# Performance work log

Hardware: AMD Instinct MI355X
Metric: run time of the kernel (lower is better)

Reference implementation:

```python
import jax, jax.numpy as jnp
import numpy as np

EPS = 1e-5

def conv2d(x, w, b=None, pad=1):
    # x: [B,C,H,W], w: [O,I,kh,kw]
    y = jax.lax.conv_general_dilated(x, w, (1, 1), [(pad, pad), (pad, pad)],
                                     dimension_numbers=('NCHW', 'OIHW', 'NCHW'))
    if b is not None:
        y = y + b[None, :, None, None]
    return y

def bn(x, g, b, m, v):
    # inference-mode batchnorm
    inv = g / jnp.sqrt(v + EPS)
    return x * inv[None, :, None, None] + (b - m * inv)[None, :, None, None]

def coord_conv(x, w, b):
    B, C, H, W = x.shape
    yy = jnp.broadcast_to(jnp.linspace(-1.0, 1.0, H)[:, None], (H, W))
    xx = jnp.broadcast_to(jnp.linspace(-1.0, 1.0, W)[None, :], (H, W))
    coords = jnp.broadcast_to(jnp.stack([xx, yy])[None], (B, 2, H, W)).astype(x.dtype)
    return conv2d(jnp.concatenate([x, coords], axis=1), w, b, pad=1)

def deform_conv(x, offset, w):
    # deformable conv v1, 3x3, pad=1, stride=1, no bias
    B, C, H, W = x.shape
    K = 9
    # offset channels interleaved (y, x) per kernel tap
    off = offset.reshape(B, K, 2, H, W)
    off_y, off_x = off[:, :, 0], off[:, :, 1]          # [B,9,H,W]
    k = jnp.arange(K)
    ko_y = (k // 3 - 1).astype(x.dtype)[None, :, None, None]
    ko_x = (k % 3 - 1).astype(x.dtype)[None, :, None, None]
    base_y = jnp.arange(H, dtype=x.dtype)[None, None, :, None]
    base_x = jnp.arange(W, dtype=x.dtype)[None, None, None, :]
    py = base_y + ko_y + off_y                          # [B,9,H,W]
    px = base_x + ko_x + off_x
    xf = x.reshape(B, C, H * W)
    y0 = jnp.floor(py)
    x0 = jnp.floor(px)
    acc = jnp.zeros((B, C, K, H, W), x.dtype)
    for dy in (0.0, 1.0):
        for dx in (0.0, 1.0):
            yy = y0 + dy
            xx = x0 + dx
            wgt = (1.0 - jnp.abs(py - yy)) * (1.0 - jnp.abs(px - xx))
            valid = (yy >= 0) & (yy < H) & (xx >= 0) & (xx < W)
            wgt = jnp.where(valid, wgt, 0.0)            # zero padding OOB
            yi = jnp.clip(yy, 0, H - 1).astype(jnp.int32)
            xi = jnp.clip(xx, 0, W - 1).astype(jnp.int32)
            idx = (yi * W + xi).reshape(B, K * H * W)
            v = jnp.take_along_axis(xf, idx[:, None, :], axis=2).reshape(B, C, K, H, W)
            acc = acc + v * wgt[:, None]
    wk = w.reshape(w.shape[0], w.shape[1], K)           # [O,I,9]
    return jnp.einsum('bckhw,ock->bohw', acc, wk)

def setup_inputs() -> dict:
    key = jax.random.key(0)
    ks = jax.random.split(key, 16)
    d_model, hd = 256, 64
    B, H, W = 8, 96, 96
    f32 = jnp.float32
    def bn_params(k):
        k1, k2, k3 = jax.random.split(k, 3)
        return (1.0 + 0.1 * jax.random.normal(k1, (hd,), f32),
                0.1 * jax.random.normal(k2, (hd,), f32),
                0.1 * jax.random.normal(k3, (hd,), f32),
                0.5 + jax.random.uniform(jax.random.fold_in(k, 7), (hd,), f32))
    bn1 = bn_params(ks[1]); bn2 = bn_params(ks[2]); bn3 = bn_params(ks[3]); bn4 = bn_params(ks[4])
    inp = {
        'features': jax.random.normal(ks[0], (B, H, W, d_model), f32),
        'coord_w': 0.05 * jax.random.normal(ks[5], (hd, d_model + 2, 3, 3), f32),
        'coord_b': jnp.zeros((hd,), f32),
        'bn1_g': bn1[0], 'bn1_b': bn1[1], 'bn1_m': bn1[2], 'bn1_v': bn1[3],
        'off_w': 0.01 * jax.random.normal(ks[6], (18, hd, 3, 3), f32),
        'off_b': 0.01 * jax.random.normal(ks[7], (18,), f32),
        'dc_w': 0.05 * jax.random.normal(ks[8], (hd, hd, 3, 3), f32),
        'bn2_g': bn2[0], 'bn2_b': bn2[1], 'bn2_m': bn2[2], 'bn2_v': bn2[3],
        'r1_w': 0.05 * jax.random.normal(ks[9], (hd, hd, 3, 3), f32),
        'bn3_g': bn3[0], 'bn3_b': bn3[1], 'bn3_m': bn3[2], 'bn3_v': bn3[3],
        'r2_w': 0.05 * jax.random.normal(ks[10], (hd, hd, 3, 3), f32),
        'bn4_g': bn4[0], 'bn4_b': bn4[1], 'bn4_m': bn4[2], 'bn4_v': bn4[3],
        'out_w': 0.1 * jax.random.normal(ks[11], (1, hd, 1, 1), f32),
        'out_b': jnp.zeros((1,), f32),
    }
    return inp

def reference(features, coord_w, coord_b, bn1_g, bn1_b, bn1_m, bn1_v,
              off_w, off_b, dc_w, bn2_g, bn2_b, bn2_m, bn2_v,
              r1_w, bn3_g, bn3_b, bn3_m, bn3_v,
              r2_w, bn4_g, bn4_b, bn4_m, bn4_v, out_w, out_b):
    x = jnp.transpose(features, (0, 3, 1, 2))           # NHWC -> NCHW
    x = jax.nn.relu(bn(coord_conv(x, coord_w, coord_b), bn1_g, bn1_b, bn1_m, bn1_v))
    offset = conv2d(x, off_w, off_b, pad=1)
    x = deform_conv(x, offset, dc_w)
    x = jax.nn.relu(bn(x, bn2_g, bn2_b, bn2_m, bn2_v))
    x = jax.nn.relu(bn(conv2d(x, r1_w, None, pad=1), bn3_g, bn3_b, bn3_m, bn3_v))
    x = jax.nn.relu(bn(conv2d(x, r2_w, None, pad=1), bn4_g, bn4_b, bn4_m, bn4_v))
    return jax.nn.sigmoid(conv2d(x, out_w, out_b, pad=0))
```

## Files before the change

### kernel.cpp

```cpp
#include <hip/hip_runtime.h>


typedef unsigned short u16;
typedef unsigned int u32;
typedef __attribute__((ext_vector_type(8)))  short bf16x8;
typedef __attribute__((ext_vector_type(16))) float f32x16;

#define EPSBN 1e-5f

__device__ __forceinline__ u16 f2bf(float f) {
  u32 u = __builtin_bit_cast(u32, f);
  u32 r = u + 0x7FFFu + ((u >> 16) & 1u);
  return (u16)(r >> 16);
}
__device__ __forceinline__ u32 pk2(float a, float b) {
  return (u32)f2bf(a) | ((u32)f2bf(b) << 16);
}
__device__ __forceinline__ float lo2f(u32 w) { return __builtin_bit_cast(float, w << 16); }
__device__ __forceinline__ float hi2f(u32 w) { return __builtin_bit_cast(float, w & 0xFFFF0000u); }

#define N_WCF 147456
#define N_WCC 9216
#define N_WOF 18432
#define N_W64 36864
#define N_ALLW (N_WCF + N_WCC + N_WOF + 3*N_W64)

__global__ __launch_bounds__(256) void prep_kernel(
    const float* __restrict__ coord_w, const float* __restrict__ off_w,
    const float* __restrict__ dc_w, const float* __restrict__ r1_w,
    const float* __restrict__ r2_w,
    u16* __restrict__ wcf, u16* __restrict__ wcc, u16* __restrict__ wof,
    u16* __restrict__ wdf, u16* __restrict__ wr1, u16* __restrict__ wr2)
{
  int i = blockIdx.x * 256 + threadIdx.x;
  if (i >= N_ALLW) return;
  int d = i;
  if (d < N_WCF) {
    int j = d & 7, lane = (d >> 3) & 63, frag = d >> 9;
    int nt = frag & 1, h = (frag >> 1) & 3, tap = (frag >> 3) % 9, cc = (frag >> 3) / 9;
    int ic = cc * 64 + h * 16 + ((lane >> 5) << 3) + j;
    int oc = nt * 32 + (lane & 31);
    wcf[d] = f2bf(coord_w[((size_t)oc * 258 + ic) * 9 + tap]);
    return;
  }
  d -= N_WCF;
  if (d < N_WCC) {
    int j = d & 7, lane = (d >> 3) & 63, frag = d >> 9;
    int nt = frag & 1, tap = frag >> 1;
    int ic = 256 + ((lane >> 5) << 3) + j;
    int oc = nt * 32 + (lane & 31);
    wcc[d] = (ic < 258) ? f2bf(coord_w[((size_t)oc * 258 + ic) * 9 + tap]) : (u16)0;
    return;
  }
  d -= N_WCC;
  if (d < N_WOF) {
    int j = d & 7, lane = (d >> 3) & 63, frag = d >> 9;
    int h = frag & 3, tap = frag >> 2;
    int ic = h * 16 + ((lane >> 5) << 3) + j;
    int oc = lane & 31;
    wof[d] = (oc < 18) ? f2bf(off_w[((size_t)oc * 64 + ic) * 9 + tap]) : (u16)0;
    return;
  }
  d -= N_WOF;
  int seg = d / N_W64;
  int e = d - seg * N_W64;
  int j = e & 7, lane = (e >> 3) & 63, frag = e >> 9;
  int nt = frag & 1, h = (frag >> 1) & 3, tap = frag >> 3;
  int ic = h * 16 + ((lane >> 5) << 3) + j;
  int oc = nt * 32 + (lane & 31);
  const float* src = (seg == 0) ? dc_w : (seg == 1) ? r1_w : r2_w;
  u16* dst = (seg == 0) ? wdf : (seg == 1) ? wr1 : wr2;
  dst[e] = f2bf(src[((size_t)oc * 64 + ic) * 9 + tap]);
}

__global__ __launch_bounds__(256, 3) void coord_conv_kernel(
    const float* __restrict__ feat, const u16* __restrict__ wcf,
    const u16* __restrict__ wcc, const float* __restrict__ cb,
    const float* __restrict__ g, const float* __restrict__ bb,
    const float* __restrict__ m, const float* __restrict__ v,
    u16* __restrict__ x1b)
{
  __shared__ __align__(16) u16 tile[6 * 34 * 72];
  const int t = threadIdx.x;
  const int wv = t >> 6, lane = t & 63;
  const int l31 = lane & 31, l5 = lane >> 5;
  const int x0 = blockIdx.x * 32, y0 = blockIdx.y * 4, b = blockIdx.z;

  f32x16 acc[2] = {};
  float4 pa[7], pb[7];

  auto issue = [&](int cc) {
    #pragma unroll
    for (int r = 0; r < 7; ++r) {
      const int i = t + r * 256;
      const float4 z = {0.f, 0.f, 0.f, 0.f};
      pa[r] = z; pb[r] = z;
      if (i < 1632) {
        const int px = i >> 3, gg = i & 7;
        const int ly = px / 34, lx = px - ly * 34;
        const int gy = y0 + ly - 1, gx = x0 + lx - 1;
        if ((unsigned)gy < 96u && (unsigned)gx < 96u) {
          const float* p = feat + ((size_t)((b * 96 + gy) * 96 + gx)) * 256
                           + cc * 64 + gg * 8;
          pa[r] = *(const float4*)p;
          pb[r] = *(const float4*)(p + 4);
        }
      }
    }
  };
  auto commit = [&]() {
    #pragma unroll
    for (int r = 0; r < 7; ++r) {
      const int i = t + r * 256;
      if (i < 1632) {
        const int px = i >> 3, gg = i & 7;
        uint4 o;
        o.x = pk2(pa[r].x, pa[r].y); o.y = pk2(pa[r].z, pa[r].w);
        o.z = pk2(pb[r].x, pb[r].y); o.w = pk2(pb[r].z, pb[r].w);
        *(uint4*)(tile + px * 72 + gg * 8) = o;
      }
    }
  };

  issue(0);
  for (int cc = 0; cc < 4; ++cc) {
    __syncthreads();
    commit();
    __syncthreads();
    if (cc < 3) issue(cc + 1);
    #pragma unroll
    for (int tap = 0; tap < 9; ++tap) {
      const int dy = tap / 3, dx = tap - dy * 3;
      #pragma unroll
      for (int h = 0; h < 4; ++h) {
        const bf16x8 afr = *(const bf16x8*)(tile +
            ((wv + dy) * 34 + l31 + dx) * 72 + h * 16 + l5 * 8);
        #pragma unroll
        for (int nt = 0; nt < 2; ++nt) {
          const bf16x8 bfr = *(const bf16x8*)(wcf +
              ((size_t)((((cc * 9 + tap) * 4 + h) * 2) + nt)) * 512 + lane * 8);
          acc[nt] = __builtin_amdgcn_mfma_f32_32x32x16_bf16(afr, bfr, acc[nt],
                                                            0, 0, 0);
        }
      }
    }
  }

  __syncthreads();
  for (int i = t; i < 408; i += 256) {
    const int px = i >> 1, gg = i & 1;
    const int ly = px / 34, lx = px - ly * 34;
    const int gy = y0 + ly - 1, gx = x0 + lx - 1;
    uint4 o = {0u, 0u, 0u, 0u};
    if (gg == 0 && (unsigned)gy < 96u && (unsigned)gx < 96u) {
      const float xx = -1.f + (2.f / 95.f) * (float)gx;
      const float yy = -1.f + (2.f / 95.f) * (float)gy;
      o.x = pk2(xx, yy);
    }
    *(uint4*)(tile + (ly * 34 + lx) * 72 + gg * 8) = o;
  }
  __syncthreads();
  #pragma unroll
  for (int tap = 0; tap < 9; ++tap) {
    const int dy = tap / 3, dx = tap - dy * 3;
    const bf16x8 afr = *(const bf16x8*)(tile +
        ((wv + dy) * 34 + l31 + dx) * 72 + l5 * 8);
    #pragma unroll
    for (int nt = 0; nt < 2; ++nt) {
      const bf16x8 bfr = *(const bf16x8*)(wcc +
          ((size_t)(tap * 2 + nt)) * 512 + lane * 8);
      acc[nt] = __builtin_amdgcn_mfma_f32_32x32x16_bf16(afr, bfr, acc[nt],
                                                        0, 0, 0);
    }
  }

  const int y = y0 + wv;
  #pragma unroll
  for (int nt = 0; nt < 2; ++nt) {
    const int oc = nt * 32 + l31;
    const float inv = g[oc] * rsqrtf(v[oc] + EPSBN);
    const float sh = bb[oc] - m[oc] * inv + cb[oc] * inv;
    #pragma unroll
    for (int r = 0; r < 16; ++r) {
      const int xr = (r & 3) + 8 * (r >> 2) + 4 * l5;
      const float val = fmaxf(fmaf(acc[nt][r], inv, sh), 0.f);
      x1b[((size_t)((b * 96 + y) * 96 + x0 + xr)) * 64 + oc] = f2bf(val);
    }
  }
}

template<int NN, int EPI>
__global__ __launch_bounds__(256, 4) void conv64_kernel(
    const u16* __restrict__ xin, const u16* __restrict__ wf,
    const float* __restrict__ bias,
    const float* __restrict__ g, const float* __restrict__ bb,
    const float* __restrict__ m, const float* __restrict__ v,
    const float* __restrict__ ow, const float* __restrict__ ob,
    void* __restrict__ outp)
{
  __shared__ __align__(16) u16 tile[6 * 34 * 72];
  __shared__ float red[128];
  const int t = threadIdx.x;
  const int wv = t >> 6, lane = t & 63;
  const int l31 = lane & 31, l5 = lane >> 5;
  const int x0 = blockIdx.x * 32, y0 = blockIdx.y * 4, b = blockIdx.z;

  uint4 pf[7];
  #pragma unroll
  for (int r = 0; r < 7; ++r) {
    const int i = t + r * 256;
    const uint4 z = {0u, 0u, 0u, 0u};
    pf[r] = z;
    if (i < 1632) {
      const int px = i >> 3, gg = i & 7;
      const int ly = px / 34, lx = px - ly * 34;
      const int gy = y0 + ly - 1, gx = x0 + lx - 1;
      if ((unsigned)gy < 96u && (unsigned)gx < 96u)
        pf[r] = *(const uint4*)(xin + (((size_t)((b * 96 + gy) * 96 + gx)) << 6)
                                + gg * 8);
    }
  }
  #pragma unroll
  for (int r = 0; r < 7; ++r) {
    const int i = t + r * 256;
    if (i < 1632) {
      const int px = i >> 3, gg = i & 7;
      *(uint4*)(tile + px * 72 + gg * 8) = pf[r];
    }
  }
  __syncthreads();

  f32x16 acc[NN] = {};
  #pragma unroll
  for (int tap = 0; tap < 9; ++tap) {
    const int dy = tap / 3, dx = tap - dy * 3;
    #pragma unroll
    for (int h = 0; h < 4; ++h) {
      const bf16x8 afr = *(const bf16x8*)(tile +
          ((wv + dy) * 34 + l31 + dx) * 72 + h * 16 + l5 * 8);
      #pragma unroll
      for (int nt = 0; nt < NN; ++nt) {
        const bf16x8 bfr = *(const bf16x8*)(wf +
            ((size_t)((tap * 4 + h) * NN + nt)) * 512 + lane * 8);
        acc[nt] = __builtin_amdgcn_mfma_f32_32x32x16_bf16(afr, bfr, acc[nt],
                                                          0, 0, 0);
      }
    }
  }

  const int y = y0 + wv;
  if constexpr (EPI == 0) {
    u16* xo = (u16*)outp;
    #pragma unroll
    for (int nt = 0; nt < NN; ++nt) {
      const int oc = nt * 32 + l31;
      const float inv = g[oc] * rsqrtf(v[oc] + EPSBN);
      const float sh = bb[oc] - m[oc] * inv;
      #pragma unroll
      for (int r = 0; r < 16; ++r) {
        const int xr = (r & 3) + 8 * (r >> 2) + 4 * l5;
        const float val = fmaxf(fmaf(acc[nt][r], inv, sh), 0.f);
        xo[((size_t)((b * 96 + y) * 96 + x0 + xr)) * 64 + oc] = f2bf(val);
      }
    }
  } else if constexpr (EPI == 1) {
    float* fo = (float*)outp;
    const int oc = l31;
    if (oc < 18) {
      const float bs = bias[oc];
      #pragma unroll
      for (int r = 0; r < 16; ++r) {
        const int xr = (r & 3) + 8 * (r >> 2) + 4 * l5;
        fo[((size_t)((b * 96 + y) * 96 + x0 + xr)) * 18 + oc] = acc[0][r] + bs;
      }
    }
  } else {
    float pr[16];
    #pragma unroll
    for (int r = 0; r < 16; ++r) pr[r] = 0.f;
    #pragma unroll
    for (int nt = 0; nt < NN; ++nt) {
      const int oc = nt * 32 + l31;
      const float inv = g[oc] * rsqrtf(v[oc] + EPSBN);
      const float sh = bb[oc] - m[oc] * inv;
      const float wo = ow[oc];
      #pragma unroll
      for (int r = 0; r < 16; ++r) {
        const float val = fmaxf(fmaf(acc[nt][r], inv, sh), 0.f);
        pr[r] = fmaf(val, wo, pr[r]);
      }
    }
    #pragma unroll
    for (int mask = 1; mask <= 16; mask <<= 1)
      #pragma unroll
      for (int r = 0; r < 16; ++r)
        pr[r] += __shfl_xor(pr[r], mask);
    if (l31 == 0) {
      #pragma unroll
      for (int r = 0; r < 16; ++r) {
        const int xr = (r & 3) + 8 * (r >> 2) + 4 * l5;
        red[wv * 32 + xr] = pr[r];
      }
    }
    __syncthreads();
    if (t < 128) {
      float* fo = (float*)outp;
      const int yy = y0 + (t >> 5), xx = x0 + (t & 31);
      const float val = red[t] + ob[0];
      fo[(size_t)(b * 96 + yy) * 96 + xx] = 1.f / (1.f + expf(-val));
    }
  }
}

__global__ __launch_bounds__(256, 4) void deform_kernel(
    const u16* __restrict__ x1b, const float* __restrict__ off,
    const u16* __restrict__ wdf,
    const float* __restrict__ g, const float* __restrict__ bb,
    const float* __restrict__ m, const float* __restrict__ v,
    u16* __restrict__ x2b)
{
  __shared__ __align__(16) u16 s[128 * 72];
  __shared__ float offs[128 * 18];
  const int t = threadIdx.x;
  const int wv = t >> 6, lane = t & 63;
  const int l31 = lane & 31, l5 = lane >> 5;
  const int x0 = blockIdx.x * 16, y0 = blockIdx.y * 8, b = blockIdx.z;

  {
    float po[9];
    #pragma unroll
    for (int r = 0; r < 9; ++r) {
      const int i = t + r * 256;
      const int p = i / 18, c = i - p * 18;
      const int gy = y0 + (p >> 4), gx = x0 + (p & 15);
      po[r] = off[((size_t)((b * 96 + gy) * 96 + gx)) * 18 + c];
    }
    #pragma unroll
    for (int r = 0; r < 9; ++r) offs[t + r * 256] = po[r];
  }

  f32x16 acc[2] = {};

  for (int k = 0; k < 9; ++k) {
    __syncthreads();
    #pragma unroll
    for (int rr = 0; rr < 2; ++rr) {
      const int role = t + rr * 256;
      const int sp = role >> 2, part = role & 3;
      const int sy = y0 + (sp >> 4), sx = x0 + (sp & 15);
      const float oy = offs[sp * 18 + 2 * k];
      const float ox = offs[sp * 18 + 2 * k + 1];
      const float py = (float)(sy + k / 3 - 1) + oy;
      const float px = (float)(sx + k % 3 - 1) + ox;
      const float yf = floorf(py), xf = floorf(px);
      const float fy = py - yf, fx = px - xf;
      const int yi = (int)yf, xi = (int)xf;
      float val[16];
      #pragma unroll
      for (int j = 0; j < 16; ++j) val[j] = 0.f;
      #pragma unroll
      for (int cor = 0; cor < 4; ++cor) {
        const int cy = yi + (cor >> 1), cx = xi + (cor & 1);
        if ((unsigned)cy < 96u && (unsigned)cx < 96u) {
          const float wy = (cor & 2) ? fy : 1.f - fy;
          const float wx = (cor & 1) ? fx : 1.f - fx;
          const float wgt = wy * wx;
          const u16* sp2 = x1b + ((size_t)((b * 96 + cy) * 96 + cx)) * 64
                           + part * 16;
          const uint4 ua = *(const uint4*)sp2;
          const uint4 ub = *(const uint4*)(sp2 + 8);
          const u32 uu[8] = {ua.x, ua.y, ua.z, ua.w, ub.x, ub.y, ub.z, ub.w};
          #pragma unroll
          for (int u = 0; u < 8; ++u) {
            val[2 * u]     = fmaf(wgt, lo2f(uu[u]), val[2 * u]);
            val[2 * u + 1] = fmaf(wgt, hi2f(uu[u]), val[2 * u + 1]);
          }
        }
      }
      u32 pk[8];
      #pragma unroll
      for (int u = 0; u < 8; ++u) pk[u] = pk2(val[2 * u], val[2 * u + 1]);
      uint4 w0 = {pk[0], pk[1], pk[2], pk[3]};
      uint4 w1 = {pk[4], pk[5], pk[6], pk[7]};
      *(uint4*)(s + sp * 72 + part * 16) = w0;
      *(uint4*)(s + sp * 72 + part * 16 + 8) = w1;
    }
    __syncthreads();
    #pragma unroll
    for (int h = 0; h < 4; ++h) {
      const bf16x8 afr = *(const bf16x8*)(s + (wv * 32 + l31) * 72
                                          + h * 16 + l5 * 8);
      #pragma unroll
      for (int nt = 0; nt < 2; ++nt) {
        const bf16x8 bfr = *(const bf16x8*)(wdf +
            ((size_t)((k * 4 + h) * 2 + nt)) * 512 + lane * 8);
        acc[nt] = __builtin_amdgcn_mfma_f32_32x32x16_bf16(afr, bfr, acc[nt],
                                                          0, 0, 0);
      }
    }
  }

  #pragma unroll
  for (int nt = 0; nt < 2; ++nt) {
    const int oc = nt * 32 + l31;
    const float inv = g[oc] * rsqrtf(v[oc] + EPSBN);
    const float sh = bb[oc] - m[oc] * inv;
    #pragma unroll
    for (int r = 0; r < 16; ++r) {
      const int pxi = wv * 32 + (r & 3) + 8 * (r >> 2) + 4 * l5;
      const int y = y0 + (pxi >> 4), x = x0 + (pxi & 15);
      const float val = fmaxf(fmaf(acc[nt][r], inv, sh), 0.f);
      x2b[((size_t)((b * 96 + y) * 96 + x)) * 64 + oc] = f2bf(val);
    }
  }
}

extern "C" void kernel_launch(void* const* d_in, const int* in_sizes, int n_in,
                              void* d_out, int out_size, void* d_ws,
                              size_t ws_size, hipStream_t stream)
{
  (void)in_sizes; (void)n_in; (void)out_size; (void)ws_size;
  const float* features = (const float*)d_in[0];
  const float* coord_w  = (const float*)d_in[1];
  const float* coord_b  = (const float*)d_in[2];
  const float* bn1g = (const float*)d_in[3];
  const float* bn1b = (const float*)d_in[4];
  const float* bn1m = (const float*)d_in[5];
  const float* bn1v = (const float*)d_in[6];
  const float* off_w = (const float*)d_in[7];
  const float* off_b = (const float*)d_in[8];
  const float* dc_w  = (const float*)d_in[9];
  const float* bn2g = (const float*)d_in[10];
  const float* bn2b = (const float*)d_in[11];
  const float* bn2m = (const float*)d_in[12];
  const float* bn2v = (const float*)d_in[13];
  const float* r1_w = (const float*)d_in[14];
  const float* bn3g = (const float*)d_in[15];
  const float* bn3b = (const float*)d_in[16];
  const float* bn3m = (const float*)d_in[17];
  const float* bn3v = (const float*)d_in[18];
  const float* r2_w = (const float*)d_in[19];
  const float* bn4g = (const float*)d_in[20];
  const float* bn4b = (const float*)d_in[21];
  const float* bn4m = (const float*)d_in[22];
  const float* bn4v = (const float*)d_in[23];
  const float* out_w = (const float*)d_in[24];
  const float* out_b = (const float*)d_in[25];

  char* W = (char*)d_ws;
  float* offb = (float*)W;
  u16*   x1b  = (u16*)(W + 5308416);
  u16*   x2b  = (u16*)(W + 14745600);
  u16*   x3b  = (u16*)(W + 24182784);
  u16*   wcf  = (u16*)(W + 33619968);
  u16*   wcc  = wcf + N_WCF;
  u16*   wof  = wcc + N_WCC;
  u16*   wdf  = wof + N_WOF;
  u16*   wr1  = wdf + N_W64;
  u16*   wr2  = wr1 + N_W64;

  prep_kernel<<<(N_ALLW + 255) / 256, 256, 0, stream>>>(
      coord_w, off_w, dc_w, r1_w, r2_w, wcf, wcc, wof, wdf, wr1, wr2);

  dim3 grid(3, 24, 8);
  dim3 gridD(6, 12, 8);

  coord_conv_kernel<<<grid, 256, 0, stream>>>(
      features, wcf, wcc, coord_b, bn1g, bn1b, bn1m, bn1v, x1b);
  conv64_kernel<1, 1><<<grid, 256, 0, stream>>>(
      x1b, wof, off_b, nullptr, nullptr, nullptr, nullptr, nullptr, nullptr,
      (void*)offb);
  deform_kernel<<<gridD, 256, 0, stream>>>(
      x1b, offb, wdf, bn2g, bn2b, bn2m, bn2v, x2b);
  conv64_kernel<2, 0><<<grid, 256, 0, stream>>>(
      x2b, wr1, nullptr, bn3g, bn3b, bn3m, bn3v, nullptr, nullptr, (void*)x3b);
  conv64_kernel<2, 2><<<grid, 256, 0, stream>>>(
      x3b, wr2, nullptr, bn4g, bn4b, bn4m, bn4v, out_w, out_b, d_out);
}
```

Baseline: 259.7 us.

## Double wavefronts per block, split output channels across waves, pipeline deform gathers

```diff
diff --git a/kernel.cpp b/kernel.cpp
--- a/kernel.cpp
+++ b/kernel.cpp
@@ -73,7 +73,7 @@
   dst[e] = f2bf(src[((size_t)oc * 64 + ic) * 9 + tap]);
 }
 
-__global__ __launch_bounds__(256, 3) void coord_conv_kernel(
+__global__ __launch_bounds__(512, 4) void coord_conv_kernel(
     const float* __restrict__ feat, const u16* __restrict__ wcf,
     const u16* __restrict__ wcc, const float* __restrict__ cb,
     const float* __restrict__ g, const float* __restrict__ bb,
@@ -84,15 +84,16 @@
   const int t = threadIdx.x;
   const int wv = t >> 6, lane = t & 63;
   const int l31 = lane & 31, l5 = lane >> 5;
+  const int row = wv & 3, ntw = wv >> 2;
   const int x0 = blockIdx.x * 32, y0 = blockIdx.y * 4, b = blockIdx.z;
 
-  f32x16 acc[2] = {};
-  float4 pa[7], pb[7];
+  f32x16 acc = {};
+  float4 pa[4], pb[4];
 
   auto issue = [&](int cc) {
     #pragma unroll
-    for (int r = 0; r < 7; ++r) {
-      const int i = t + r * 256;
+    for (int r = 0; r < 4; ++r) {
+      const int i = t + r * 512;
       const float4 z = {0.f, 0.f, 0.f, 0.f};
       pa[r] = z; pb[r] = z;
       if (i < 1632) {
@@ -110,8 +111,8 @@
   };
   auto commit = [&]() {
     #pragma unroll
-    for (int r = 0; r < 7; ++r) {
-      const int i = t + r * 256;
+    for (int r = 0; r < 4; ++r) {
+      const int i = t + r * 512;
       if (i < 1632) {
         const int px = i >> 3, gg = i & 7;
         uint4 o;
@@ -134,20 +135,16 @@
       #pragma unroll
       for (int h = 0; h < 4; ++h) {
         const bf16x8 afr = *(const bf16x8*)(tile +
-            ((wv + dy) * 34 + l31 + dx) * 72 + h * 16 + l5 * 8);
-        #pragma unroll
-        for (int nt = 0; nt < 2; ++nt) {
-          const bf16x8 bfr = *(const bf16x8*)(wcf +
-              ((size_t)((((cc * 9 + tap) * 4 + h) * 2) + nt)) * 512 + lane * 8);
-          acc[nt] = __builtin_amdgcn_mfma_f32_32x32x16_bf16(afr, bfr, acc[nt],
-                                                            0, 0, 0);
-        }
+            ((row + dy) * 34 + l31 + dx) * 72 + h * 16 + l5 * 8);
+        const bf16x8 bfr = *(const bf16x8*)(wcf +
+            ((size_t)((((cc * 9 + tap) * 4 + h) * 2) + ntw)) * 512 + lane * 8);
+        acc = __builtin_amdgcn_mfma_f32_32x32x16_bf16(afr, bfr, acc, 0, 0, 0);
       }
     }
   }
 
   __syncthreads();
-  for (int i = t; i < 408; i += 256) {
+  for (int i = t; i < 408; i += 512) {
     const int px = i >> 1, gg = i & 1;
     const int ly = px / 34, lx = px - ly * 34;
     const int gy = y0 + ly - 1, gx = x0 + lx - 1;
@@ -164,33 +161,26 @@
   for (int tap = 0; tap < 9; ++tap) {
     const int dy = tap / 3, dx = tap - dy * 3;
     const bf16x8 afr = *(const bf16x8*)(tile +
-        ((wv + dy) * 34 + l31 + dx) * 72 + l5 * 8);
-    #pragma unroll
-    for (int nt = 0; nt < 2; ++nt) {
-      const bf16x8 bfr = *(const bf16x8*)(wcc +
-          ((size_t)(tap * 2 + nt)) * 512 + lane * 8);
-      acc[nt] = __builtin_amdgcn_mfma_f32_32x32x16_bf16(afr, bfr, acc[nt],
-                                                        0, 0, 0);
-    }
-  }
-
-  const int y = y0 + wv;
+        ((row + dy) * 34 + l31 + dx) * 72 + l5 * 8);
+    const bf16x8 bfr = *(const bf16x8*)(wcc +
+        ((size_t)(tap * 2 + ntw)) * 512 + lane * 8);
+    acc = __builtin_amdgcn_mfma_f32_32x32x16_bf16(afr, bfr, acc, 0, 0, 0);
+  }
+
+  const int y = y0 + row;
+  const int oc = ntw * 32 + l31;
+  const float inv = g[oc] * rsqrtf(v[oc] + EPSBN);
+  const float sh = bb[oc] - m[oc] * inv + cb[oc] * inv;
   #pragma unroll
-  for (int nt = 0; nt < 2; ++nt) {
-    const int oc = nt * 32 + l31;
-    const float inv = g[oc] * rsqrtf(v[oc] + EPSBN);
-    const float sh = bb[oc] - m[oc] * inv + cb[oc] * inv;
-    #pragma unroll
-    for (int r = 0; r < 16; ++r) {
-      const int xr = (r & 3) + 8 * (r >> 2) + 4 * l5;
-      const float val = fmaxf(fmaf(acc[nt][r], inv, sh), 0.f);
-      x1b[((size_t)((b * 96 + y) * 96 + x0 + xr)) * 64 + oc] = f2bf(val);
-    }
+  for (int r = 0; r < 16; ++r) {
+    const int xr = (r & 3) + 8 * (r >> 2) + 4 * l5;
+    const float val = fmaxf(fmaf(acc[r], inv, sh), 0.f);
+    x1b[((size_t)((b * 96 + y) * 96 + x0 + xr)) * 64 + oc] = f2bf(val);
   }
 }
 
 template<int NN, int EPI>
-__global__ __launch_bounds__(256, 4) void conv64_kernel(
+__global__ __launch_bounds__(512, 4) void conv64_kernel(
     const u16* __restrict__ xin, const u16* __restrict__ wf,
     const float* __restrict__ bias,
     const float* __restrict__ g, const float* __restrict__ bb,
@@ -199,16 +189,17 @@
     void* __restrict__ outp)
 {
   __shared__ __align__(16) u16 tile[6 * 34 * 72];
-  __shared__ float red[128];
+  __shared__ float red[2][128];
   const int t = threadIdx.x;
   const int wv = t >> 6, lane = t & 63;
   const int l31 = lane & 31, l5 = lane >> 5;
+  const int row = wv & 3, ntw = wv >> 2;
   const int x0 = blockIdx.x * 32, y0 = blockIdx.y * 4, b = blockIdx.z;
 
-  uint4 pf[7];
+  uint4 pf[4];
   #pragma unroll
-  for (int r = 0; r < 7; ++r) {
-    const int i = t + r * 256;
+  for (int r = 0; r < 4; ++r) {
+    const int i = t + r * 512;
     const uint4 z = {0u, 0u, 0u, 0u};
     pf[r] = z;
     if (i < 1632) {
@@ -221,8 +212,8 @@
     }
   }
   #pragma unroll
-  for (int r = 0; r < 7; ++r) {
-    const int i = t + r * 256;
+  for (int r = 0; r < 4; ++r) {
+    const int i = t + r * 512;
     if (i < 1632) {
       const int px = i >> 3, gg = i & 7;
       *(uint4*)(tile + px * 72 + gg * 8) = pf[r];
@@ -230,63 +221,80 @@
   }
   __syncthreads();
 
-  f32x16 acc[NN] = {};
+  f32x16 acc = {};
   #pragma unroll
   for (int tap = 0; tap < 9; ++tap) {
     const int dy = tap / 3, dx = tap - dy * 3;
-    #pragma unroll
-    for (int h = 0; h < 4; ++h) {
-      const bf16x8 afr = *(const bf16x8*)(tile +
-          ((wv + dy) * 34 + l31 + dx) * 72 + h * 16 + l5 * 8);
-      #pragma unroll
-      for (int nt = 0; nt < NN; ++nt) {
+    if constexpr (NN == 2) {
+      #pragma unroll
+      for (int h = 0; h < 4; ++h) {
+        const bf16x8 afr = *(const bf16x8*)(tile +
+            ((row + dy) * 34 + l31 + dx) * 72 + h * 16 + l5 * 8);
         const bf16x8 bfr = *(const bf16x8*)(wf +
-            ((size_t)((tap * 4 + h) * NN + nt)) * 512 + lane * 8);
-        acc[nt] = __builtin_amdgcn_mfma_f32_32x32x16_bf16(afr, bfr, acc[nt],
-                                                          0, 0, 0);
-      }
-    }
-  }
-
-  const int y = y0 + wv;
+            ((size_t)((tap * 4 + h) * 2 + ntw)) * 512 + lane * 8);
+        acc = __builtin_amdgcn_mfma_f32_32x32x16_bf16(afr, bfr, acc, 0, 0, 0);
+      }
+    } else {
+      #pragma unroll
+      for (int hh = 0; hh < 2; ++hh) {
+        const int h = ntw * 2 + hh;
+        const bf16x8 afr = *(const bf16x8*)(tile +
+            ((row + dy) * 34 + l31 + dx) * 72 + h * 16 + l5 * 8);
+        const bf16x8 bfr = *(const bf16x8*)(wf +
+            ((size_t)(tap * 4 + h)) * 512 + lane * 8);
+        acc = __builtin_amdgcn_mfma_f32_32x32x16_bf16(afr, bfr, acc, 0, 0, 0);
+      }
+    }
+  }
+
+  const int y = y0 + row;
   if constexpr (EPI == 0) {
     u16* xo = (u16*)outp;
-    #pragma unroll
-    for (int nt = 0; nt < NN; ++nt) {
-      const int oc = nt * 32 + l31;
-      const float inv = g[oc] * rsqrtf(v[oc] + EPSBN);
-      const float sh = bb[oc] - m[oc] * inv;
-      #pragma unroll
-      for (int r = 0; r < 16; ++r) {
-        const int xr = (r & 3) + 8 * (r >> 2) + 4 * l5;
-        const float val = fmaxf(fmaf(acc[nt][r], inv, sh), 0.f);
-        xo[((size_t)((b * 96 + y) * 96 + x0 + xr)) * 64 + oc] = f2bf(val);
-      }
+    const int oc = ntw * 32 + l31;
+    const float inv = g[oc] * rsqrtf(v[oc] + EPSBN);
+    const float sh = bb[oc] - m[oc] * inv;
+    #pragma unroll
+    for (int r = 0; r < 16; ++r) {
+      const int xr = (r & 3) + 8 * (r >> 2) + 4 * l5;
+      const float val = fmaxf(fmaf(acc[r], inv, sh), 0.f);
+      xo[((size_t)((b * 96 + y) * 96 + x0 + xr)) * 64 + oc] = f2bf(val);
     }
   } else if constexpr (EPI == 1) {
-    float* fo = (float*)outp;
-    const int oc = l31;
-    if (oc < 18) {
-      const float bs = bias[oc];
-      #pragma unroll
-      for (int r = 0; r < 16; ++r) {
-        const int xr = (r & 3) + 8 * (r >> 2) + 4 * l5;
-        fo[((size_t)((b * 96 + y) * 96 + x0 + xr)) * 18 + oc] = acc[0][r] + bs;
+    __syncthreads();
+    float* redk = (float*)tile;
+    if (ntw == 1) {
+      #pragma unroll
+      for (int r = 0; r < 16; ++r)
+        redk[r * 256 + row * 64 + lane] = acc[r];
+    }
+    __syncthreads();
+    if (ntw == 0) {
+      #pragma unroll
+      for (int r = 0; r < 16; ++r)
+        acc[r] += redk[r * 256 + row * 64 + lane];
+      float* fo = (float*)outp;
+      const int oc = l31;
+      if (oc < 18) {
+        const float bs = bias[oc];
+        #pragma unroll
+        for (int r = 0; r < 16; ++r) {
+          const int xr = (r & 3) + 8 * (r >> 2) + 4 * l5;
+          fo[((size_t)((b * 96 + y) * 96 + x0 + xr)) * 18 + oc] = acc[r] + bs;
+        }
       }
     }
   } else {
     float pr[16];
     #pragma unroll
     for (int r = 0; r < 16; ++r) pr[r] = 0.f;
-    #pragma unroll
-    for (int nt = 0; nt < NN; ++nt) {
-      const int oc = nt * 32 + l31;
+    {
+      const int oc = ntw * 32 + l31;
       const float inv = g[oc] * rsqrtf(v[oc] + EPSBN);
       const float sh = bb[oc] - m[oc] * inv;
       const float wo = ow[oc];
       #pragma unroll
       for (int r = 0; r < 16; ++r) {
-        const float val = fmaxf(fmaf(acc[nt][r], inv, sh), 0.f);
+        const float val = fmaxf(fmaf(acc[r], inv, sh), 0.f);
         pr[r] = fmaf(val, wo, pr[r]);
       }
     }
@@ -299,119 +307,141 @@
       #pragma unroll
       for (int r = 0; r < 16; ++r) {
         const int xr = (r & 3) + 8 * (r >> 2) + 4 * l5;
-        red[wv * 32 + xr] = pr[r];
+        red[ntw][row * 32 + xr] = pr[r];
       }
     }
     __syncthreads();
     if (t < 128) {
       float* fo = (float*)outp;
       const int yy = y0 + (t >> 5), xx = x0 + (t & 31);
-      const float val = red[t] + ob[0];
+      const float val = red[0][t] + red[1][t] + ob[0];
       fo[(size_t)(b * 96 + yy) * 96 + xx] = 1.f / (1.f + expf(-val));
     }
   }
 }
 
-__global__ __launch_bounds__(256, 4) void deform_kernel(
+__global__ __launch_bounds__(512, 4) void deform_kernel(
     const u16* __restrict__ x1b, const float* __restrict__ off,
     const u16* __restrict__ wdf,
     const float* __restrict__ g, const float* __restrict__ bb,
     const float* __restrict__ m, const float* __restrict__ v,
     u16* __restrict__ x2b)
 {
-  __shared__ __align__(16) u16 s[128 * 72];
+  __shared__ __align__(16) u16 s[2 * 128 * 72];
   __shared__ float offs[128 * 18];
   const int t = threadIdx.x;
   const int wv = t >> 6, lane = t & 63;
   const int l31 = lane & 31, l5 = lane >> 5;
+  const int mt = wv & 3, ntw = wv >> 2;
   const int x0 = blockIdx.x * 16, y0 = blockIdx.y * 8, b = blockIdx.z;
 
   {
-    float po[9];
-    #pragma unroll
-    for (int r = 0; r < 9; ++r) {
-      const int i = t + r * 256;
-      const int p = i / 18, c = i - p * 18;
-      const int gy = y0 + (p >> 4), gx = x0 + (p & 15);
-      po[r] = off[((size_t)((b * 96 + gy) * 96 + gx)) * 18 + c];
-    }
-    #pragma unroll
-    for (int r = 0; r < 9; ++r) offs[t + r * 256] = po[r];
-  }
-
-  f32x16 acc[2] = {};
+    float po[5];
+    #pragma unroll
+    for (int r = 0; r < 5; ++r) {
+      const int i = t + r * 512;
+      po[r] = 0.f;
+      if (i < 2304) {
+        const int p = i / 18, c = i - p * 18;
+        const int gy = y0 + (p >> 4), gx = x0 + (p & 15);
+        po[r] = off[((size_t)((b * 96 + gy) * 96 + gx)) * 18 + c];
+      }
+    }
+    #pragma unroll
+    for (int r = 0; r < 5; ++r) {
+      const int i = t + r * 512;
+      if (i < 2304) offs[i] = po[r];
+    }
+  }
+  __syncthreads();
+
+  const int sp = t >> 2, part = t & 3;
+  const int sy = y0 + (sp >> 4), sx = x0 + (sp & 15);
+
+  uint4 gbuf[8];
+  float w4[4];
+
+  auto prefetch = [&](int k) {
+    const float oy = offs[sp * 18 + 2 * k];
+    const float ox = offs[sp * 18 + 2 * k + 1];
+    const float py = (float)(sy + k / 3 - 1) + oy;
+    const float px = (float)(sx + k % 3 - 1) + ox;
+    const float yf = floorf(py), xf = floorf(px);
+    const float fy = py - yf, fx = px - xf;
+    const int yi = (int)yf, xi = (int)xf;
+    #pragma unroll
+    for (int cor = 0; cor < 4; ++cor) {
+      const int cy = yi + (cor >> 1), cx = xi + (cor & 1);
+      const uint4 z = {0u, 0u, 0u, 0u};
+      gbuf[2 * cor] = z; gbuf[2 * cor + 1] = z;
+      const float wy = (cor & 2) ? fy : 1.f - fy;
+      const float wx = (cor & 1) ? fx : 1.f - fx;
+      w4[cor] = 0.f;
+      if ((unsigned)cy < 96u && (unsigned)cx < 96u) {
+        w4[cor] = wy * wx;
+        const u16* p = x1b + ((size_t)((b * 96 + cy) * 96 + cx)) * 64
+                       + part * 16;
+        gbuf[2 * cor]     = *(const uint4*)p;
+        gbuf[2 * cor + 1] = *(const uint4*)(p + 8);
+      }
+    }
+  };
+  auto combine = [&](u16* dst) {
+    float val[16];
+    #pragma unroll
+    for (int j = 0; j < 16; ++j) val[j] = 0.f;
+    #pragma unroll
+    for (int cor = 0; cor < 4; ++cor) {
+      const float wgt = w4[cor];
+      const u32 uu[8] = {gbuf[2 * cor].x, gbuf[2 * cor].y,
+                         gbuf[2 * cor].z, gbuf[2 * cor].w,
+                         gbuf[2 * cor + 1].x, gbuf[2 * cor + 1].y,
+                         gbuf[2 * cor + 1].z, gbuf[2 * cor + 1].w};
+      #pragma unroll
+      for (int u = 0; u < 8; ++u) {
+        val[2 * u]     = fmaf(wgt, lo2f(uu[u]), val[2 * u]);
+        val[2 * u + 1] = fmaf(wgt, hi2f(uu[u]), val[2 * u + 1]);
+      }
+    }
+    u32 pk[8];
+    #pragma unroll
+    for (int u = 0; u < 8; ++u) pk[u] = pk2(val[2 * u], val[2 * u + 1]);
+    uint4 w0 = {pk[0], pk[1], pk[2], pk[3]};
+    uint4 w1 = {pk[4], pk[5], pk[6], pk[7]};
+    *(uint4*)(dst + sp * 72 + part * 16) = w0;
+    *(uint4*)(dst + sp * 72 + part * 16 + 8) = w1;
+  };
+
+  f32x16 acc = {};
+
+  prefetch(0);
+  combine(s);
+  __syncthreads();
 
   for (int k = 0; k < 9; ++k) {
+    u16* cur = s + (k & 1) * 9216;
+    if (k < 8) prefetch(k + 1);
+    #pragma unroll
+    for (int h = 0; h < 4; ++h) {
+      const bf16x8 afr = *(const bf16x8*)(cur + (mt * 32 + l31) * 72
+                                          + h * 16 + l5 * 8);
+      const bf16x8 bfr = *(const bf16x8*)(wdf +
+          ((size_t)((k * 4 + h) * 2 + ntw)) * 512 + lane * 8);
+      acc = __builtin_amdgcn_mfma_f32_32x32x16_bf16(afr, bfr, acc, 0, 0, 0);
+    }
+    if (k < 8) combine(s + ((k + 1) & 1) * 9216);
     __syncthreads();
-    #pragma unroll
-    for (int rr = 0; rr < 2; ++rr) {
-      const int role = t + rr * 256;
-      const int sp = role >> 2, part = role & 3;
-      const int sy = y0 + (sp >> 4), sx = x0 + (sp & 15);
-      const float oy = offs[sp * 18 + 2 * k];
-      const float ox = offs[sp * 18 + 2 * k + 1];
-      const float py = (float)(sy + k / 3 - 1) + oy;
-      const float px = (float)(sx + k % 3 - 1) + ox;
-      const float yf = floorf(py), xf = floorf(px);
-      const float fy = py - yf, fx = px - xf;
-      const int yi = (int)yf, xi = (int)xf;
-      float val[16];
-      #pragma unroll
-      for (int j = 0; j < 16; ++j) val[j] = 0.f;
-      #pragma unroll
-      for (int cor = 0; cor < 4; ++cor) {
-        const int cy = yi + (cor >> 1), cx = xi + (cor & 1);
-        if ((unsigned)cy < 96u && (unsigned)cx < 96u) {
-          const float wy = (cor & 2) ? fy : 1.f - fy;
-          const float wx = (cor & 1) ? fx : 1.f - fx;
-          const float wgt = wy * wx;
-          const u16* sp2 = x1b + ((size_t)((b * 96 + cy) * 96 + cx)) * 64
-                           + part * 16;
-          const uint4 ua = *(const uint4*)sp2;
-          const uint4 ub = *(const uint4*)(sp2 + 8);
-          const u32 uu[8] = {ua.x, ua.y, ua.z, ua.w, ub.x, ub.y, ub.z, ub.w};
-          #pragma unroll
-          for (int u = 0; u < 8; ++u) {
-            val[2 * u]     = fmaf(wgt, lo2f(uu[u]), val[2 * u]);
-            val[2 * u + 1] = fmaf(wgt, hi2f(uu[u]), val[2 * u + 1]);
-          }
-        }
-      }
-      u32 pk[8];
-      #pragma unroll
-      for (int u = 0; u < 8; ++u) pk[u] = pk2(val[2 * u], val[2 * u + 1]);
-      uint4 w0 = {pk[0], pk[1], pk[2], pk[3]};
-      uint4 w1 = {pk[4], pk[5], pk[6], pk[7]};
-      *(uint4*)(s + sp * 72 + part * 16) = w0;
-      *(uint4*)(s + sp * 72 + part * 16 + 8) = w1;
-    }
-    __syncthreads();
-    #pragma unroll
-    for (int h = 0; h < 4; ++h) {
-      const bf16x8 afr = *(const bf16x8*)(s + (wv * 32 + l31) * 72
-                                          + h * 16 + l5 * 8);
-      #pragma unroll
-      for (int nt = 0; nt < 2; ++nt) {
-        const bf16x8 bfr = *(const bf16x8*)(wdf +
-            ((size_t)((k * 4 + h) * 2 + nt)) * 512 + lane * 8);
-        acc[nt] = __builtin_amdgcn_mfma_f32_32x32x16_bf16(afr, bfr, acc[nt],
-                                                          0, 0, 0);
-      }
-    }
-  }
-
+  }
+
+  const int oc = ntw * 32 + l31;
+  const float inv = g[oc] * rsqrtf(v[oc] + EPSBN);
+  const float sh = bb[oc] - m[oc] * inv;
   #pragma unroll
-  for (int nt = 0; nt < 2; ++nt) {
-    const int oc = nt * 32 + l31;
-    const float inv = g[oc] * rsqrtf(v[oc] + EPSBN);
-    const float sh = bb[oc] - m[oc] * inv;
-    #pragma unroll
-    for (int r = 0; r < 16; ++r) {
-      const int pxi = wv * 32 + (r & 3) + 8 * (r >> 2) + 4 * l5;
-      const int y = y0 + (pxi >> 4), x = x0 + (pxi & 15);
-      const float val = fmaxf(fmaf(acc[nt][r], inv, sh), 0.f);
-      x2b[((size_t)((b * 96 + y) * 96 + x)) * 64 + oc] = f2bf(val);
-    }
+  for (int r = 0; r < 16; ++r) {
+    const int pxi = mt * 32 + (r & 3) + 8 * (r >> 2) + 4 * l5;
+    const int y = y0 + (pxi >> 4), x = x0 + (pxi & 15);
+    const float val = fmaxf(fmaf(acc[r], inv, sh), 0.f);
+    x2b[((size_t)((b * 96 + y) * 96 + x)) * 64 + oc] = f2bf(val);
   }
 }
 
@@ -465,15 +495,15 @@
   dim3 grid(3, 24, 8);
   dim3 gridD(6, 12, 8);
 
-  coord_conv_kernel<<<grid, 256, 0, stream>>>(
+  coord_conv_kernel<<<grid, 512, 0, stream>>>(
       features, wcf, wcc, coord_b, bn1g, bn1b, bn1m, bn1v, x1b);
-  conv64_kernel<1, 1><<<grid, 256, 0, stream>>>(
+  conv64_kernel<1, 1><<<grid, 512, 0, stream>>>(
       x1b, wof, off_b, nullptr, nullptr, nullptr, nullptr, nullptr, nullptr,
       (void*)offb);
-  deform_kernel<<<gridD, 256, 0, stream>>>(
+  deform_kernel<<<gridD, 512, 0, stream>>>(
       x1b, offb, wdf, bn2g, bn2b, bn2m, bn2v, x2b);
-  conv64_kernel<2, 0><<<grid, 256, 0, stream>>>(
+  conv64_kernel<2, 0><<<grid, 512, 0, stream>>>(
       x2b, wr1, nullptr, bn3g, bn3b, bn3m, bn3v, nullptr, nullptr, (void*)x3b);
-  conv64_kernel<2, 2><<<grid, 256, 0, stream>>>(
+  conv64_kernel<2, 2><<<grid, 512, 0, stream>>>(
       x3b, wr2, nullptr, bn4g, bn4b, bn4m, bn4v, out_w, out_b, d_out);
 }
```

After: 252.6 us. -2.7%, faster.
